# Kernel tuning notes

Measured on AMD Instinct MI355X. Metric: run time of the kernel, lower is better.

The kernel has to match this reference:

```python
import jax, jax.numpy as jnp
import numpy as np

V, D, T, B, H, L, FF = 32000, 1024, 1024, 2, 16, 2, 4096


def _ln(x, g, b, eps=1e-5):
    m = x.mean(-1, keepdims=True)
    v = ((x - m) ** 2).mean(-1, keepdims=True)
    return (x - m) * jax.lax.rsqrt(v + eps) * g + b


def setup_inputs() -> dict:
    key = jax.random.key(0)
    ks = jax.random.split(key, 16)
    s = 0.02  # init scale for stable softmax/logits
    return {
        "idx": jax.random.randint(ks[0], (B, T), 0, V),
        "targets": jax.random.randint(ks[1], (B, T), 0, V),
        "word_emb": jax.random.normal(ks[2], (V, D), jnp.float32) * s,
        "pos_emb": jax.random.normal(ks[3], (T, D), jnp.float32) * s,
        "ln1_g": jnp.ones((L, D), jnp.float32),
        "ln1_b": jnp.zeros((L, D), jnp.float32),
        "wq": jax.random.normal(ks[4], (L, D, D), jnp.float32) * s,
        "wk": jax.random.normal(ks[5], (L, D, D), jnp.float32) * s,
        "wv": jax.random.normal(ks[6], (L, D, D), jnp.float32) * s,
        "proj_w": jax.random.normal(ks[7], (L, D, D), jnp.float32) * s,
        "proj_b": jnp.zeros((L, D), jnp.float32),
        "ln2_g": jnp.ones((L, D), jnp.float32),
        "ln2_b": jnp.zeros((L, D), jnp.float32),
        "ff_w1": jax.random.normal(ks[8], (L, D, FF), jnp.float32) * s,
        "ff_b1": jnp.zeros((L, FF), jnp.float32),
        "ff_w2": jax.random.normal(ks[9], (L, FF, D), jnp.float32) * s,
        "ff_b2": jnp.zeros((L, D), jnp.float32),
        "lnf_g": jnp.ones((D,), jnp.float32),
        "lnf_b": jnp.zeros((D,), jnp.float32),
        "lm_w": jax.random.normal(ks[10], (D, V), jnp.float32) * s,
        "lm_b": jnp.zeros((V,), jnp.float32),
    }


def reference(word_emb, pos_emb, ln1_g, ln1_b, wq, wk, wv, proj_w, proj_b,
              ln2_g, ln2_b, ff_w1, ff_b1, ff_w2, ff_b2, lnf_g, lnf_b,
              lm_w, lm_b, idx, targets):
    b, t = idx.shape
    d = word_emb.shape[1]
    n_layer, n_head = wq.shape[0], H
    x = word_emb[idx] + pos_emb[:t]              # [B,T,D]
    causal = jnp.tril(jnp.ones((t, t), bool))
    maps = []
    for l in range(n_layer):
        h = _ln(x, ln1_g[l], ln1_b[l])
        q = (h @ wq[l]).reshape(b, t, n_head, -1)  # [B,T,H,hd]
        k = (h @ wk[l]).reshape(b, t, n_head, -1)
        v = (h @ wv[l]).reshape(b, t, n_head, -1)
        # NOTE: source scales by n_embd**-0.5 (full embedding dim), not head_size
        wei = jnp.einsum('bqhd,bkhd->bhqk', q, k) * (d ** -0.5)
        wei = jnp.where(causal, wei, -jnp.inf)
        wei = jax.nn.softmax(wei, axis=-1)        # [B,H,T,T]
        maps.append(wei)
        att = jnp.einsum('bhqk,bkhd->bqhd', wei, v).reshape(b, t, d)
        x = x + att @ proj_w[l] + proj_b[l]
        h2 = _ln(x, ln2_g[l], ln2_b[l])
        x = x + jax.nn.relu(h2 @ ff_w1[l] + ff_b1[l]) @ ff_w2[l] + ff_b2[l]
    x = _ln(x, lnf_g, lnf_b)
    logits = (x @ lm_w + lm_b).reshape(b * t, -1)  # [B*T, V]
    logp = jax.nn.log_softmax(logits, axis=-1)
    loss = -logp[jnp.arange(b * t), targets.reshape(-1)].mean()
    probs = jax.nn.log_softmax(x, axis=-1)         # source: LogSoftmax of final-LN x
    return (logits, loss, jnp.stack(maps), probs)
```

## Files before the change

### kernel.cpp

```cpp
#include <hip/hip_runtime.h>
#include <hip/hip_bf16.h>

#define VSZ 32000
#define DM  1024
#define TSEQ 1024
#define BB  2
#define HH  16
#define LL  2
#define FFD 4096
#define NTOK (BB*TSEQ)
#define QT  16

static constexpr size_t LOGITS_OFF = 0;
static constexpr size_t LOSS_OFF   = (size_t)NTOK * VSZ;
static constexpr size_t MAPS_OFF   = LOSS_OFF + 1;
static constexpr size_t PROBS_OFF  = MAPS_OFF + (size_t)LL*BB*HH*TSEQ*TSEQ;

typedef __attribute__((ext_vector_type(8))) short bf8;
typedef __attribute__((ext_vector_type(4))) float f32x4;
typedef __attribute__((ext_vector_type(4))) short short4v;

__device__ __forceinline__ short f2bf(float f) {
  union { float f; unsigned u; } v; v.f = f;
  unsigned r = v.u + 0x7FFFu + ((v.u >> 16) & 1u);
  return (short)(r >> 16);
}
__device__ __forceinline__ float bf2f(short s) {
  union { unsigned u; float f; } v; v.u = ((unsigned)(unsigned short)s) << 16;
  return v.f;
}

__device__ __forceinline__ void gload16(const void* g, void* l) {
  __builtin_amdgcn_global_load_lds(
      (const __attribute__((address_space(1))) void*)g,
      (__attribute__((address_space(3))) void*)l, 16, 0, 0);
}

__device__ __forceinline__ float block_sum256(float v, float* sh) {
#pragma unroll
  for (int off = 32; off; off >>= 1) v += __shfl_down(v, off);
  int wid = threadIdx.x >> 6, lane = threadIdx.x & 63;
  if (lane == 0) sh[wid] = v;
  __syncthreads();
  v = sh[0] + sh[1] + sh[2] + sh[3];
  __syncthreads();
  return v;
}
__device__ __forceinline__ float block_max256(float v, float* sh) {
#pragma unroll
  for (int off = 32; off; off >>= 1) v = fmaxf(v, __shfl_down(v, off));
  int wid = threadIdx.x >> 6, lane = threadIdx.x & 63;
  if (lane == 0) sh[wid] = v;
  __syncthreads();
  v = fmaxf(fmaxf(sh[0], sh[1]), fmaxf(sh[2], sh[3]));
  __syncthreads();
  return v;
}

static constexpr size_t PLW = (size_t)4 * DM * DM + (size_t)DM * FFD + (size_t)FFD * DM;
__global__ __launch_bounds__(256) void transpose_all(const float* __restrict__ wq,
    const float* __restrict__ wk, const float* __restrict__ wv,
    const float* __restrict__ proj_w, const float* __restrict__ ff_w1,
    const float* __restrict__ ff_w2, short* __restrict__ wt_base) {
  __shared__ float T[64][65];
  const int bid = blockIdx.x;
  const int l = bid / 3072, r = bid % 3072;
  short* qbase = wt_base + (size_t)l * PLW;
  const float* W; short* Wt; int K, N, tn, tk;
  if (r < 1024) {
    int s = r >> 8, rr = r & 255;
    W = (s == 0 ? wq : (s == 1 ? wk : (s == 2 ? wv : proj_w))) + (size_t)l * DM * DM;
    Wt = qbase + (size_t)s * DM * DM;
    K = DM; N = DM; tn = rr & 15; tk = rr >> 4;
  } else if (r < 2048) {
    int rr = r - 1024;
    W = ff_w1 + (size_t)l * DM * FFD; Wt = qbase + (size_t)4 * DM * DM;
    K = DM; N = FFD; tn = rr & 63; tk = rr >> 6;
  } else {
    int rr = r - 2048;
    W = ff_w2 + (size_t)l * FFD * DM; Wt = qbase + (size_t)4 * DM * DM + (size_t)DM * FFD;
    K = FFD; N = DM; tn = rr & 15; tk = rr >> 4;
  }
  const int n0 = tn * 64, k0 = tk * 64;
  const int tid = threadIdx.x;
  const int lr = tid >> 4, lc4 = (tid & 15) * 4;
#pragma unroll
  for (int p = 0; p < 4; ++p) {
    int k = lr + p * 16;
    float4 w = *(const float4*)&W[(size_t)(k0 + k) * N + n0 + lc4];
    T[k][lc4] = w.x; T[k][lc4+1] = w.y; T[k][lc4+2] = w.z; T[k][lc4+3] = w.w;
  }
  __syncthreads();
#pragma unroll
  for (int p = 0; p < 4; ++p) {
    int n = lr + p * 16;
    short4v s;
    s.x = f2bf(T[lc4  ][n]);
    s.y = f2bf(T[lc4+1][n]);
    s.z = f2bf(T[lc4+2][n]);
    s.w = f2bf(T[lc4+3][n]);
    *(short4v*)&Wt[(size_t)(n0 + n) * K + k0 + lc4] = s;
  }
}

__global__ __launch_bounds__(256) void transpose_cvt(const float* __restrict__ W,
    short* __restrict__ Wt, int K, int N) {
  __shared__ float T[64][65];
  const int n0 = blockIdx.x * 64, k0 = blockIdx.y * 64;
  const int tid = threadIdx.x;
  const int lr = tid >> 4, lc4 = (tid & 15) * 4;
#pragma unroll
  for (int p = 0; p < 4; ++p) {
    int k = lr + p * 16;
    float4 w = *(const float4*)&W[(size_t)(k0 + k) * N + n0 + lc4];
    T[k][lc4] = w.x; T[k][lc4+1] = w.y; T[k][lc4+2] = w.z; T[k][lc4+3] = w.w;
  }
  __syncthreads();
#pragma unroll
  for (int p = 0; p < 4; ++p) {
    int n = lr + p * 16;
    short4v s;
    s.x = f2bf(T[lc4  ][n]);
    s.y = f2bf(T[lc4+1][n]);
    s.z = f2bf(T[lc4+2][n]);
    s.w = f2bf(T[lc4+3][n]);
    *(short4v*)&Wt[(size_t)(n0 + n) * K + k0 + lc4] = s;
  }
}

__global__ __launch_bounds__(256) void embed_kernel(const int* __restrict__ idx,
    const float* __restrict__ we, const float* __restrict__ pe, float* __restrict__ x) {
  int i = blockIdx.x * 256 + threadIdx.x;
  int n = i >> 10;
  int d = i & 1023;
  int t = n & (TSEQ - 1);
  x[i] = we[(size_t)idx[n] * DM + d] + pe[(size_t)t * DM + d];
}

__global__ __launch_bounds__(256) void ln_bf(const float* __restrict__ in,
    const float* __restrict__ g, const float* __restrict__ b,
    short* __restrict__ outb) {
  __shared__ float sh[4];
  int row = blockIdx.x, tid = threadIdx.x;
  const float* xr = in + (size_t)row * DM;
  float4 v = *(const float4*)&xr[tid * 4];
  float s  = v.x + v.y + v.z + v.w;
  float s2 = v.x*v.x + v.y*v.y + v.z*v.z + v.w*v.w;
  s  = block_sum256(s, sh);
  s2 = block_sum256(s2, sh);
  float mean = s * (1.0f / DM);
  float var  = s2 * (1.0f / DM) - mean * mean;
  float inv  = rsqrtf(var + 1e-5f);
  float4 gv = *(const float4*)&g[tid * 4];
  float4 bv = *(const float4*)&b[tid * 4];
  float4 o;
  o.x = (v.x - mean) * inv * gv.x + bv.x;
  o.y = (v.y - mean) * inv * gv.y + bv.y;
  o.z = (v.z - mean) * inv * gv.z + bv.z;
  o.w = (v.w - mean) * inv * gv.w + bv.w;
  short4v ob;
  ob.x = f2bf(o.x); ob.y = f2bf(o.y); ob.z = f2bf(o.z); ob.w = f2bf(o.w);
  *(short4v*)&outb[(size_t)row * DM + tid * 4] = ob;
}

__global__ __launch_bounds__(256) void ln_probs(const float* __restrict__ in,
    const float* __restrict__ g, const float* __restrict__ b,
    short* __restrict__ outb, float* __restrict__ probs) {
  __shared__ float sh[4];
  int row = blockIdx.x, tid = threadIdx.x;
  const float* xr = in + (size_t)row * DM;
  float4 v = *(const float4*)&xr[tid * 4];
  float s  = v.x + v.y + v.z + v.w;
  float s2 = v.x*v.x + v.y*v.y + v.z*v.z + v.w*v.w;
  s  = block_sum256(s, sh);
  s2 = block_sum256(s2, sh);
  float mean = s * (1.0f / DM);
  float var  = s2 * (1.0f / DM) - mean * mean;
  float inv  = rsqrtf(var + 1e-5f);
  float4 gv = *(const float4*)&g[tid * 4];
  float4 bv = *(const float4*)&b[tid * 4];
  float4 o;
  o.x = (v.x - mean) * inv * gv.x + bv.x;
  o.y = (v.y - mean) * inv * gv.y + bv.y;
  o.z = (v.z - mean) * inv * gv.z + bv.z;
  o.w = (v.w - mean) * inv * gv.w + bv.w;
  short4v ob;
  ob.x = f2bf(o.x); ob.y = f2bf(o.y); ob.z = f2bf(o.z); ob.w = f2bf(o.w);
  *(short4v*)&outb[(size_t)row * DM + tid * 4] = ob;
  float m = block_max256(fmaxf(fmaxf(o.x, o.y), fmaxf(o.z, o.w)), sh);
  float ssum = __expf(o.x-m) + __expf(o.y-m) + __expf(o.z-m) + __expf(o.w-m);
  ssum = block_sum256(ssum, sh);
  float lg = m + logf(ssum);
  float* orow = probs + (size_t)row * DM + tid * 4;
  orow[0] = o.x - lg;
  orow[1] = o.y - lg;
  orow[2] = o.z - lg;
  orow[3] = o.w - lg;
}

template<int BIAS, int RES, int RELU, int OUTBF, int LOSSP, int SWZ>
__global__ __launch_bounds__(256) void gemm_bb(const short* __restrict__ A, int lda,
    const short* __restrict__ Bt, const float* __restrict__ bias,
    void* __restrict__ Cv, int M, int K, int Nn,
    float* __restrict__ lpart, int mblocks) {
  __shared__ short As[128 * 32];
  __shared__ short Bs[128 * 32];
  float* Cf = (float*)Cv;
  short* Cb = (short*)Cv;
  const int tid  = threadIdx.x;
  int bm, bn;
  if (SWZ) {
    const int cpx = gridDim.x >> 3;
    const int swz = (blockIdx.x & 7) * cpx + (blockIdx.x >> 3);
    bm = (swz % mblocks) * 128;
    bn = (swz / mblocks) * 128;
  } else {
    bm = blockIdx.x * 128; bn = blockIdx.y * 128;
  }
  const int lane = tid & 63, wid = tid >> 6;
  const int wr = wid >> 1, wc = wid & 1;
  const int lr = lane & 15, lg = lane >> 4;
  const int srow = lane >> 2;
  const int schunk = (lane & 3) * 8;

  f32x4 acc[4][4];
#pragma unroll
  for (int i = 0; i < 4; ++i)
#pragma unroll
    for (int j = 0; j < 4; ++j) acc[i][j] = (f32x4)0.f;

  for (int k0 = 0; k0 < K; k0 += 32) {
#pragma unroll
    for (int t = 0; t < 2; ++t) {
      const int issue = wid * 2 + t;
      const int row = issue * 16 + srow;
      gload16(&A[(size_t)(bm + row) * lda + k0 + schunk], &As[issue * 512]);
      gload16(&Bt[(size_t)(bn + row) * K  + k0 + schunk], &Bs[issue * 512]);
    }
    __syncthreads();
    bf8 af[4], bfv[4];
#pragma unroll
    for (int i = 0; i < 4; ++i)
      af[i] = *(const bf8*)&As[(wr * 64 + i * 16 + lr) * 32 + lg * 8];
#pragma unroll
    for (int j = 0; j < 4; ++j)
      bfv[j] = *(const bf8*)&Bs[(wc * 64 + j * 16 + lr) * 32 + lg * 8];
#pragma unroll
    for (int i = 0; i < 4; ++i)
#pragma unroll
      for (int j = 0; j < 4; ++j)
        acc[i][j] = __builtin_amdgcn_mfma_f32_16x16x32_bf16(af[i], bfv[j], acc[i][j], 0, 0, 0);
    __syncthreads();
  }
  float* Ls = (float*)As;
#pragma unroll
  for (int i = 0; i < 4; ++i) {
#pragma unroll
    for (int v = 0; v < 4; ++v) {
      int rl = wr * 64 + i * 16 + lg * 4 + v;
      size_t rowb = (size_t)(bm + rl) * Nn;
      float pe = 0.f;
#pragma unroll
      for (int j = 0; j < 4; ++j) {
        int col = bn + wc * 64 + j * 16 + lr;
        float val = acc[i][j][v];
        if (BIAS) val += bias[col];
        if (RES)  val += Cf[rowb + col];
        if (RELU) val = fmaxf(val, 0.f);
        if (OUTBF) Cb[rowb + col] = f2bf(val);
        else       Cf[rowb + col] = val;
        if (LOSSP) pe += __expf(val);
      }
      if (LOSSP) {
#pragma unroll
        for (int off = 8; off; off >>= 1) pe += __shfl_xor(pe, off);
        if (lr == 0) Ls[rl * 2 + wc] = pe;
      }
    }
  }
  if (LOSSP) {
    __syncthreads();
    if (tid < 128)
      lpart[(size_t)(bm + tid) * 256 + (bn >> 7)] = Ls[tid * 2] + Ls[tid * 2 + 1];
  }
}

template<int BIAS, int LOSSP, int SWZ>
__global__ __launch_bounds__(256) void gemm_lm_cvt(const short* __restrict__ A,
    const float* __restrict__ Bw, const float* __restrict__ bias,
    float* __restrict__ C, int M, int K, int Nn,
    float* __restrict__ lpart, int mblocks) {
  __shared__ short As[128 * 40];
  __shared__ short Bs[128 * 40];
  const int tid  = threadIdx.x;
  int bm, bn;
  if (SWZ) {
    const int cpx = gridDim.x >> 3;
    const int swz = (blockIdx.x & 7) * cpx + (blockIdx.x >> 3);
    bm = (swz % mblocks) * 128;
    bn = (swz / mblocks) * 128;
  } else {
    bm = blockIdx.x * 128; bn = blockIdx.y * 128;
  }
  const int lane = tid & 63, wid = tid >> 6;
  const int wr = wid >> 1, wc = wid & 1;
  const int lr = lane & 15, lg = lane >> 4;
  const int sr = tid >> 1, sh2 = (tid & 1) * 16;
  const int sbn = tid & 127, sbk = (tid >> 7) * 16;
  f32x4 acc[4][4];
#pragma unroll
  for (int i = 0; i < 4; ++i)
#pragma unroll
    for (int j = 0; j < 4; ++j) acc[i][j] = (f32x4)0.f;
  for (int k0 = 0; k0 < K; k0 += 32) {
    {
      const short* asrc = &A[(size_t)(bm + sr) * K + k0 + sh2];
      *(bf8*)&As[sr * 40 + sh2    ] = *(const bf8*)&asrc[0];
      *(bf8*)&As[sr * 40 + sh2 + 8] = *(const bf8*)&asrc[8];
    }
    {
      short tmp[16];
#pragma unroll
      for (int e = 0; e < 16; ++e)
        tmp[e] = f2bf(Bw[(size_t)(k0 + sbk + e) * Nn + bn + sbn]);
      *(bf8*)&Bs[sbn * 40 + sbk    ] = *(bf8*)&tmp[0];
      *(bf8*)&Bs[sbn * 40 + sbk + 8] = *(bf8*)&tmp[8];
    }
    __syncthreads();
    bf8 af[4], bfv[4];
#pragma unroll
    for (int i = 0; i < 4; ++i)
      af[i] = *(const bf8*)&As[(wr * 64 + i * 16 + lr) * 40 + lg * 8];
#pragma unroll
    for (int j = 0; j < 4; ++j)
      bfv[j] = *(const bf8*)&Bs[(wc * 64 + j * 16 + lr) * 40 + lg * 8];
#pragma unroll
    for (int i = 0; i < 4; ++i)
#pragma unroll
      for (int j = 0; j < 4; ++j)
        acc[i][j] = __builtin_amdgcn_mfma_f32_16x16x32_bf16(af[i], bfv[j], acc[i][j], 0, 0, 0);
    __syncthreads();
  }
  float* Ls = (float*)As;
#pragma unroll
  for (int i = 0; i < 4; ++i) {
#pragma unroll
    for (int v = 0; v < 4; ++v) {
      int rl = wr * 64 + i * 16 + lg * 4 + v;
      size_t rowb = (size_t)(bm + rl) * Nn;
      float pe = 0.f;
#pragma unroll
      for (int j = 0; j < 4; ++j) {
        int col = bn + wc * 64 + j * 16 + lr;
        float val = acc[i][j][v];
        if (BIAS) val += bias[col];
        C[rowb + col] = val;
        if (LOSSP) pe += __expf(val);
      }
      if (LOSSP) {
#pragma unroll
        for (int off = 8; off; off >>= 1) pe += __shfl_xor(pe, off);
        if (lr == 0) Ls[rl * 2 + wc] = pe;
      }
    }
  }
  if (LOSSP) {
    __syncthreads();
    if (tid < 128)
      lpart[(size_t)(bm + tid) * 256 + (bn >> 7)] = Ls[tid * 2] + Ls[tid * 2 + 1];
  }
}

__global__ __launch_bounds__(256) void attn_fused(const short* __restrict__ qkv_bf,
    float* __restrict__ maps_l, short* __restrict__ att_bf) {
  __shared__ float S[QT][1032];
  __shared__ short Qs[QT * 72];
  __shared__ short Ks[64 * 72];
  const int tid = threadIdx.x;
  const int q0 = blockIdx.x * QT;
  const int bh = blockIdx.y;
  const int b = bh >> 4, h = bh & 15;
  const int lane = tid & 63, wid = tid >> 6;
  const int lr = lane & 15, lg = lane >> 4;
  if (tid < 128) {
    int r = tid >> 3, c8 = (tid & 7) * 8;
    *(bf8*)&Qs[r * 72 + c8] =
      *(const bf8*)&qkv_bf[(size_t)(b * TSEQ + q0 + r) * 3072 + h * 64 + c8];
  }
  const int ktmax = (q0 + QT - 1) / 64 + 1;
  for (int kt = 0; kt < ktmax; ++kt) {
    const int k0 = kt * 64;
    {
      int r = tid >> 2, c16 = (tid & 3) * 16;
      const short* src = &qkv_bf[(size_t)(b * TSEQ + k0 + r) * 3072 + 1024 + h * 64 + c16];
      *(bf8*)&Ks[r * 72 + c16    ] = *(const bf8*)&src[0];
      *(bf8*)&Ks[r * 72 + c16 + 8] = *(const bf8*)&src[8];
    }
    __syncthreads();
    f32x4 acc = (f32x4)0.f;
#pragma unroll
    for (int ds = 0; ds < 2; ++ds) {
      bf8 af  = *(const bf8*)&Qs[lr * 72 + ds * 32 + lg * 8];
      bf8 bfv = *(const bf8*)&Ks[(wid * 16 + lr) * 72 + ds * 32 + lg * 8];
      acc = __builtin_amdgcn_mfma_f32_16x16x32_bf16(af, bfv, acc, 0, 0, 0);
    }
#pragma unroll
    for (int v = 0; v < 4; ++v)
      S[lg * 4 + v][k0 + wid * 16 + lr] = acc[v] * 0.03125f;
    __syncthreads();
  }
  const int r = tid >> 4, l16 = tid & 15;
  const int qg = q0 + r;
  float m = -1e30f;
  for (int c = l16; c <= qg; c += 16) m = fmaxf(m, S[r][c]);
#pragma unroll
  for (int off = 8; off; off >>= 1) m = fmaxf(m, __shfl_xor(m, off, 16));
  float ssum = 0.f;
  for (int c = l16; c <= qg; c += 16) ssum += __expf(S[r][c] - m);
#pragma unroll
  for (int off = 8; off; off >>= 1) ssum += __shfl_xor(ssum, off, 16);
  const float inv = 1.f / ssum;
  float* mrow = maps_l + (size_t)bh * TSEQ * TSEQ + (size_t)qg * TSEQ;
  for (int c = l16; c < TSEQ; c += 16) {
    float p = 0.f;
    if (c <= qg) { p = __expf(S[r][c] - m) * inv; S[r][c] = p; }
    mrow[c] = p;
  }
  __syncthreads();
  const int dbase = l16 * 4;
  float4 a = {0.f, 0.f, 0.f, 0.f};
  for (int kt = 0; kt < ktmax; ++kt) {
    const int k0 = kt * 64;
    {
      int vr2 = tid >> 2, vc2 = (tid & 3) * 16;
      const short* src = &qkv_bf[(size_t)(b * TSEQ + k0 + vr2) * 3072 + 2048 + h * 64 + vc2];
      *(bf8*)&Ks[vr2 * 72 + vc2    ] = *(const bf8*)&src[0];
      *(bf8*)&Ks[vr2 * 72 + vc2 + 8] = *(const bf8*)&src[8];
    }
    __syncthreads();
    int kend = qg - k0 + 1;
    if (kend > 64) kend = 64;
    for (int k = 0; k < kend; ++k) {
      float p = S[r][k0 + k];
      short4v vv = *(const short4v*)&Ks[k * 72 + dbase];
      a.x += p * bf2f(vv.x); a.y += p * bf2f(vv.y);
      a.z += p * bf2f(vv.z); a.w += p * bf2f(vv.w);
    }
    __syncthreads();
  }
  short* orow = &att_bf[(size_t)(b * TSEQ + qg) * DM + h * 64 + dbase];
  short4v s0;
  s0.x = f2bf(a.x); s0.y = f2bf(a.y); s0.z = f2bf(a.z); s0.w = f2bf(a.w);
  *(short4v*)orow = s0;
}

__global__ __launch_bounds__(256) void loss_final(const float* __restrict__ lpart,
    const float* __restrict__ logits, const int* __restrict__ targets,
    float* __restrict__ rowloss) {
  __shared__ float sh[4];
  int row = blockIdx.x, tid = threadIdx.x;
  float s = (tid < VSZ / 128) ? lpart[(size_t)row * 256 + tid] : 0.f;
  s = block_sum256(s, sh);
  if (tid == 0)
    rowloss[row] = logf(s) - logits[(size_t)row * VSZ + targets[row]];
}
__global__ __launch_bounds__(256) void loss_reduce(const float* __restrict__ rowloss,
    float* __restrict__ out) {
  __shared__ float sh[4];
  float s = 0.f;
  for (int i = threadIdx.x; i < NTOK; i += 256) s += rowloss[i];
  s = block_sum256(s, sh);
  if (threadIdx.x == 0) out[0] = s * (1.0f / NTOK);
}

extern "C" void kernel_launch(void* const* d_in, const int* in_sizes, int n_in,
                              void* d_out, int out_size, void* d_ws, size_t ws_size,
                              hipStream_t stream) {
  const int*   idx      = (const int*)  d_in[0];
  const int*   targets  = (const int*)  d_in[1];
  const float* word_emb = (const float*)d_in[2];
  const float* pos_emb  = (const float*)d_in[3];
  const float* ln1_g    = (const float*)d_in[4];
  const float* ln1_b    = (const float*)d_in[5];
  const float* wq       = (const float*)d_in[6];
  const float* wk       = (const float*)d_in[7];
  const float* wv       = (const float*)d_in[8];
  const float* proj_w   = (const float*)d_in[9];
  const float* proj_b   = (const float*)d_in[10];
  const float* ln2_g    = (const float*)d_in[11];
  const float* ln2_b    = (const float*)d_in[12];
  const float* ff_w1    = (const float*)d_in[13];
  const float* ff_b1    = (const float*)d_in[14];
  const float* ff_w2    = (const float*)d_in[15];
  const float* ff_b2    = (const float*)d_in[16];
  const float* lnf_g    = (const float*)d_in[17];
  const float* lnf_b    = (const float*)d_in[18];
  const float* lm_w     = (const float*)d_in[19];
  const float* lm_b     = (const float*)d_in[20];

  float* outf   = (float*)d_out;
  float* logits = outf + LOGITS_OFF;
  float* lossp  = outf + LOSS_OFF;
  float* maps   = outf + MAPS_OFF;
  float* probs  = outf + PROBS_OFF;

  const size_t ND = (size_t)NTOK * DM;
  float* x    = (float*)d_ws;
  float* rowloss = x + ND;
  float* lpart   = rowloss + NTOK;
  short* qkv_bf = (short*)(lpart + (size_t)NTOK * 256);
  short* h_bf   = qkv_bf + 3 * ND;
  short* att_bf = h_bf + ND;
  short* ffh_bf = att_bf + ND;
  short* xf_bf  = ffh_bf + (size_t)NTOK * FFD;
  char*  ws_end = (char*)(xf_bf + ND);
  const size_t act_bytes = (size_t)(ws_end - (char*)d_ws);
  const size_t lmwt_bytes = (size_t)VSZ * DM * sizeof(short);
  const int lm_fast = (ws_size >= act_bytes + lmwt_bytes);
  short* lm_wt = (short*)ws_end;

  short* wt_base = (short*)logits;
  auto layer_wt = [&](int l) { return wt_base + (size_t)l * PLW; };

  dim3 b256(256);
  transpose_all<<<dim3(2 * 3072), b256, 0, stream>>>(wq, wk, wv, proj_w, ff_w1, ff_w2, wt_base);
  if (lm_fast)
    transpose_cvt<<<dim3(VSZ/64, 16), b256, 0, stream>>>(lm_w, lm_wt, DM, VSZ);

  embed_kernel<<<dim3((NTOK * DM) / 256), b256, 0, stream>>>(idx, word_emb, pos_emb, x);

  for (int l = 0; l < LL; ++l) {
    short* qkvt = layer_wt(l);
    short* projt = qkvt + (size_t)3 * DM * DM;
    short* ff1t  = projt + (size_t)DM * DM;
    short* ff2t  = ff1t + (size_t)DM * FFD;
    ln_bf<<<dim3(NTOK), b256, 0, stream>>>(x, ln1_g + l * DM, ln1_b + l * DM, h_bf);
    gemm_bb<0,0,0,1,0,0><<<dim3(NTOK/128, 3072/128), b256, 0, stream>>>(h_bf, DM, qkvt, nullptr, qkv_bf, NTOK, DM, 3072, nullptr, 0);
    float* maps_l = maps + (size_t)l * BB * HH * TSEQ * TSEQ;
    attn_fused<<<dim3(TSEQ/QT, BB*HH), b256, 0, stream>>>(qkv_bf, maps_l, att_bf);
    gemm_bb<1,1,0,0,0,0><<<dim3(NTOK/128, DM/128), b256, 0, stream>>>(att_bf, DM, projt, proj_b + l * DM, x, NTOK, DM, DM, nullptr, 0);
    ln_bf<<<dim3(NTOK), b256, 0, stream>>>(x, ln2_g + l * DM, ln2_b + l * DM, h_bf);
    gemm_bb<1,0,1,1,0,0><<<dim3(NTOK/128, FFD/128), b256, 0, stream>>>(h_bf, DM, ff1t, ff_b1 + l * FFD, ffh_bf, NTOK, DM, FFD, nullptr, 0);
    gemm_bb<1,1,0,0,0,0><<<dim3(NTOK/128, DM/128), b256, 0, stream>>>(ffh_bf, FFD, ff2t, ff_b2 + l * DM, x, NTOK, FFD, DM, nullptr, 0);
  }

  ln_probs<<<dim3(NTOK), b256, 0, stream>>>(x, lnf_g, lnf_b, xf_bf, probs);
  const int mblocks = NTOK / 128;
  const int nwg_lm = mblocks * (VSZ / 128);
  if (lm_fast)
    gemm_bb<1,0,0,0,1,1><<<dim3(nwg_lm), b256, 0, stream>>>(xf_bf, DM, lm_wt, lm_b, logits, NTOK, DM, VSZ, lpart, mblocks);
  else
    gemm_lm_cvt<1,1,1><<<dim3(nwg_lm), b256, 0, stream>>>(xf_bf, lm_w, lm_b, logits, NTOK, DM, VSZ, lpart, mblocks);
  loss_final<<<dim3(NTOK), b256, 0, stream>>>(lpart, logits, targets, rowloss);
  loss_reduce<<<dim3(1), b256, 0, stream>>>(rowloss, lossp);

  (void)in_sizes; (void)n_in; (void)out_size;
}
```

Baseline: 1.158 ms.

## Coalesce attention map stores and use swizzled 1D grid for all GEMMs

The attention kernel now normalizes probabilities in shared memory first, then writes each map row with all 256 threads issuing float4 stores across the full 1024-column row. Before, 16 lanes per row wrote scalar floats, so the dominant 268MB maps write is now wide and coalesced. The layer GEMMs switch to the 1D swizzled grid mode already used by the LM head, aiming at better L2 reuse of weight tiles. The PV loop also gets a clamped trip count and an unroll hint. The cost is an extra barrier plus a pass that re-reads shared memory.

```diff
diff --git a/kernel.cpp b/kernel.cpp
--- a/kernel.cpp
+++ b/kernel.cpp
@@ -420,11 +420,19 @@
 #pragma unroll
   for (int off = 8; off; off >>= 1) ssum += __shfl_xor(ssum, off, 16);
   const float inv = 1.f / ssum;
-  float* mrow = maps_l + (size_t)bh * TSEQ * TSEQ + (size_t)qg * TSEQ;
-  for (int c = l16; c < TSEQ; c += 16) {
-    float p = 0.f;
-    if (c <= qg) { p = __expf(S[r][c] - m) * inv; S[r][c] = p; }
-    mrow[c] = p;
+  for (int c = l16; c <= qg; c += 16)
+    S[r][c] = __expf(S[r][c] - m) * inv;
+  __syncthreads();
+  const int c4 = tid * 4;
+#pragma unroll 4
+  for (int rr = 0; rr < QT; ++rr) {
+    const int qgr = q0 + rr;
+    float4 p4;
+    p4.x = (c4     <= qgr) ? S[rr][c4    ] : 0.f;
+    p4.y = (c4 + 1 <= qgr) ? S[rr][c4 + 1] : 0.f;
+    p4.z = (c4 + 2 <= qgr) ? S[rr][c4 + 2] : 0.f;
+    p4.w = (c4 + 3 <= qgr) ? S[rr][c4 + 3] : 0.f;
+    *(float4*)&maps_l[(size_t)bh * TSEQ * TSEQ + (size_t)qgr * TSEQ + c4] = p4;
   }
   __syncthreads();
   const int dbase = l16 * 4;
@@ -440,6 +448,8 @@
     __syncthreads();
     int kend = qg - k0 + 1;
     if (kend > 64) kend = 64;
+    if (kend < 0) kend = 0;
+#pragma unroll 4
     for (int k = 0; k < kend; ++k) {
       float p = S[r][k0 + k];
       short4v vv = *(const short4v*)&Ks[k * 72 + dbase];
@@ -529,28 +539,28 @@
 
   embed_kernel<<<dim3((NTOK * DM) / 256), b256, 0, stream>>>(idx, word_emb, pos_emb, x);
 
+  const int mb = NTOK / 128;
   for (int l = 0; l < LL; ++l) {
     short* qkvt = layer_wt(l);
     short* projt = qkvt + (size_t)3 * DM * DM;
     short* ff1t  = projt + (size_t)DM * DM;
     short* ff2t  = ff1t + (size_t)DM * FFD;
     ln_bf<<<dim3(NTOK), b256, 0, stream>>>(x, ln1_g + l * DM, ln1_b + l * DM, h_bf);
-    gemm_bb<0,0,0,1,0,0><<<dim3(NTOK/128, 3072/128), b256, 0, stream>>>(h_bf, DM, qkvt, nullptr, qkv_bf, NTOK, DM, 3072, nullptr, 0);
+    gemm_bb<0,0,0,1,0,1><<<dim3(mb * (3072/128)), b256, 0, stream>>>(h_bf, DM, qkvt, nullptr, qkv_bf, NTOK, DM, 3072, nullptr, mb);
     float* maps_l = maps + (size_t)l * BB * HH * TSEQ * TSEQ;
     attn_fused<<<dim3(TSEQ/QT, BB*HH), b256, 0, stream>>>(qkv_bf, maps_l, att_bf);
-    gemm_bb<1,1,0,0,0,0><<<dim3(NTOK/128, DM/128), b256, 0, stream>>>(att_bf, DM, projt, proj_b + l * DM, x, NTOK, DM, DM, nullptr, 0);
+    gemm_bb<1,1,0,0,0,1><<<dim3(mb * (DM/128)), b256, 0, stream>>>(att_bf, DM, projt, proj_b + l * DM, x, NTOK, DM, DM, nullptr, mb);
     ln_bf<<<dim3(NTOK), b256, 0, stream>>>(x, ln2_g + l * DM, ln2_b + l * DM, h_bf);
-    gemm_bb<1,0,1,1,0,0><<<dim3(NTOK/128, FFD/128), b256, 0, stream>>>(h_bf, DM, ff1t, ff_b1 + l * FFD, ffh_bf, NTOK, DM, FFD, nullptr, 0);
-    gemm_bb<1,1,0,0,0,0><<<dim3(NTOK/128, DM/128), b256, 0, stream>>>(ffh_bf, FFD, ff2t, ff_b2 + l * DM, x, NTOK, FFD, DM, nullptr, 0);
+    gemm_bb<1,0,1,1,0,1><<<dim3(mb * (FFD/128)), b256, 0, stream>>>(h_bf, DM, ff1t, ff_b1 + l * FFD, ffh_bf, NTOK, DM, FFD, nullptr, mb);
+    gemm_bb<1,1,0,0,0,1><<<dim3(mb * (DM/128)), b256, 0, stream>>>(ffh_bf, FFD, ff2t, ff_b2 + l * DM, x, NTOK, FFD, DM, nullptr, mb);
   }
 
   ln_probs<<<dim3(NTOK), b256, 0, stream>>>(x, lnf_g, lnf_b, xf_bf, probs);
-  const int mblocks = NTOK / 128;
-  const int nwg_lm = mblocks * (VSZ / 128);
+  const int nwg_lm = mb * (VSZ / 128);
   if (lm_fast)
-    gemm_bb<1,0,0,0,1,1><<<dim3(nwg_lm), b256, 0, stream>>>(xf_bf, DM, lm_wt, lm_b, logits, NTOK, DM, VSZ, lpart, mblocks);
+    gemm_bb<1,0,0,0,1,1><<<dim3(nwg_lm), b256, 0, stream>>>(xf_bf, DM, lm_wt, lm_b, logits, NTOK, DM, VSZ, lpart, mb);
   else
-    gemm_lm_cvt<1,1,1><<<dim3(nwg_lm), b256, 0, stream>>>(xf_bf, lm_w, lm_b, logits, NTOK, DM, VSZ, lpart, mblocks);
+    gemm_lm_cvt<1,1,1><<<dim3(nwg_lm), b256, 0, stream>>>(xf_bf, lm_w, lm_b, logits, NTOK, DM, VSZ, lpart, mb);
   loss_final<<<dim3(NTOK), b256, 0, stream>>>(lpart, logits, targets, rowloss);
   loss_reduce<<<dim3(1), b256, 0, stream>>>(rowloss, lossp);
 
```

After: 1.179 ms. Within noise of the previous version (+1.8%).
